# Kernel optimization log

Hardware: AMD Instinct MI355X
Metric: run time of the kernel (lower is better)

Reference implementation:

```python
import jax, jax.numpy as jnp
import numpy as np

B, T, D = 4, 2048, 1024
H = 16
DK = D // H
SCALE = 1.0 / np.sqrt(DK)
EPS_LN = 1e-5
EPS_NORM = 1e-8


def setup_inputs() -> dict:
    key = jax.random.key(0)
    ks = jax.random.split(key, 12)
    gain = 1.0 / np.sqrt(2.0)
    # xavier_uniform bound for square [D, D] weight with gain
    bound = gain * np.sqrt(6.0 / (D + D))

    def w(k):
        return jax.random.uniform(k, (D, D), jnp.float32, -bound, bound)

    return {
        "x": jax.random.normal(ks[0], (B, T, D), jnp.float32),
        "mask": jax.random.bernoulli(ks[1], 0.1, (B, T)),  # True = masked out
        "wq": w(ks[2]), "bq": jnp.zeros((D,), jnp.float32),
        "wk": w(ks[3]), "bk": jnp.zeros((D,), jnp.float32),
        "wv": w(ks[4]), "bv": jnp.zeros((D,), jnp.float32),
        "wo": w(ks[5]), "bo": jnp.zeros((D,), jnp.float32),
        "ln_g": jnp.ones((D,), jnp.float32),
        "ln_b": jnp.zeros((D,), jnp.float32),
    }


def _layernorm(x, g, b):
    mu = jnp.mean(x, axis=-1, keepdims=True)
    var = jnp.var(x, axis=-1, keepdims=True)
    return (x - mu) * jax.lax.rsqrt(var + EPS_LN) * g + b


def _l2norm(x):
    # torch F.normalize: x / clamp_min(||x||_2, eps)
    n = jnp.sqrt(jnp.sum(x * x, axis=-1, keepdims=True))
    return x / jnp.maximum(n, EPS_NORM)


def reference(x, mask, wq, bq, wk, bk, wv, bv, wo, bo, ln_g, ln_b):
    xn = _layernorm(x, ln_g, ln_b)  # q_norm applied to shared input

    def proj(w, bias):
        y = jnp.einsum("btd,ed->bte", xn, w) + bias
        return y.reshape(B, T, H, DK).transpose(0, 2, 1, 3)  # [B,H,T,DK]

    Q = _l2norm(proj(wq, bq))
    K = _l2norm(proj(wk, bk))
    V = proj(wv, bv)

    scores = jnp.einsum("bhqd,bhkd->bhqk", Q, K) * SCALE
    scores = jnp.clip(scores, -10.0, 10.0)
    scores = jnp.where(mask[:, None, None, :], -10000.0, scores)
    scores = scores - jnp.max(scores, axis=-1, keepdims=True)
    attn = jax.nn.softmax(scores, axis=-1)

    out = jnp.einsum("bhqk,bhkd->bhqd", attn, V)
    out = out.transpose(0, 2, 1, 3).reshape(B, T, D)
    out = jnp.einsum("btd,ed->bte", out, wo) + bo
    return out * 0.5
```

## Files before the change

kernel.cpp:

```cpp
#include <hip/hip_runtime.h>
#include <hip/hip_bf16.h>
#include <cstdint>
#include <cstddef>
#include <cstring>

typedef unsigned short u16;
typedef unsigned char u8;
typedef __attribute__((ext_vector_type(8))) short short8;
typedef __attribute__((ext_vector_type(4))) float f32x4;

#define B_    4
#define T_    2048
#define D_    1024
#define H_    16
#define DK_   64
#define QSCALE_ 0.18033688011112042f

__device__ __forceinline__ float bf2f(u16 u) {
    unsigned int x = ((unsigned int)u) << 16;
    float f; __builtin_memcpy(&f, &x, 4); return f;
}
__device__ __forceinline__ u16 f2bf(float f) {
    unsigned int x; __builtin_memcpy(&x, &f, 4);
    x += 0x7fffu + ((x >> 16) & 1u);
    return (u16)(x >> 16);
}

__global__ __launch_bounds__(256) void prep_kernel(
    const u16* __restrict__ x, const u8* __restrict__ m,
    const void* s0, const void* s1, const void* s2, const void* s3,
    const void* s4, const void* s5,
    u16* __restrict__ vecs, float* __restrict__ msk, int* flag, int n)
{
    __shared__ int tot, sbits;
    int tid = threadIdx.x;
    if (tid == 0) { tot = 0; sbits = 0; }
    __syncthreads();
    int cnt = 0;
    for (int i = tid; i < 4096; i += 256) {
        int e = (x[2 * i] >> 7) & 0xFF;
        if (e > 137 || (e >= 1 && e < 97)) cnt++;
    }
    int bits = 0;
    for (int i = tid; i < n; i += 256)
        if (m[i]) bits |= (i & 7);
    for (int o = 1; o < 64; o <<= 1) { cnt += __shfl_xor(cnt, o); bits |= __shfl_xor(bits, o); }
    if ((tid & 63) == 0) { atomicAdd(&tot, cnt); if (bits) atomicOr(&sbits, bits); }
    __syncthreads();
    int f = (tot > 1024) ? 1 : 0;
    if (tid == 0) *flag = f;
    int b = sbits;
    int stride = (b & 1) ? 1 : (b & 2) ? 2 : (b & 4) ? 4 : 8;
    for (int i = tid; i < n; i += 256)
        msk[i] = m[(size_t)i * stride] ? 0.f : 1.f;
    const void* ss[6] = {s0, s1, s2, s3, s4, s5};
    for (int t = 0; t < 6; t++) {
        const void* s = ss[t];
        for (int i = tid; i < 1024; i += 256)
            vecs[t * 1024 + i] = f ? f2bf(((const float*)s)[i]) : ((const u16*)s)[i];
    }
}

__global__ __launch_bounds__(256) void convert_w_kernel(
    const void* s0, const void* s1, const void* s2, const void* s3,
    u16* d0, u16* d1, u16* d2, u16* d3, const int* __restrict__ flag)
{
    const void* s; u16* d;
    if (blockIdx.y == 0)      { s = s0; d = d0; }
    else if (blockIdx.y == 1) { s = s1; d = d1; }
    else if (blockIdx.y == 2) { s = s2; d = d2; }
    else                      { s = s3; d = d3; }
    int i4 = blockIdx.x * 256 + threadIdx.x;
    if (*flag) {
        float4 v = ((const float4*)s)[i4];
        ushort4 o; o.x = f2bf(v.x); o.y = f2bf(v.y); o.z = f2bf(v.z); o.w = f2bf(v.w);
        ((ushort4*)d)[i4] = o;
    } else {
        ((ushort4*)d)[i4] = ((const ushort4*)s)[i4];
    }
}

__global__ __launch_bounds__(256) void ln_kernel(
    const void* __restrict__ x, const u16* __restrict__ g,
    const u16* __restrict__ be, u16* __restrict__ xn, const int* __restrict__ flag)
{
    int row = blockIdx.x;
    int t = threadIdx.x;
    float v[4];
    if (*flag) {
        float4 f4 = ((const float4*)x)[(size_t)row * 256 + t];
        v[0] = f4.x; v[1] = f4.y; v[2] = f4.z; v[3] = f4.w;
    } else {
        ushort4 uv = ((const ushort4*)x)[(size_t)row * 256 + t];
        v[0] = bf2f(uv.x); v[1] = bf2f(uv.y); v[2] = bf2f(uv.z); v[3] = bf2f(uv.w);
    }
    float s = v[0] + v[1] + v[2] + v[3];
    float q = v[0]*v[0] + v[1]*v[1] + v[2]*v[2] + v[3]*v[3];
    for (int o = 1; o < 64; o <<= 1) { s += __shfl_xor(s, o); q += __shfl_xor(q, o); }
    __shared__ float rs[4], rq[4];
    int wv = t >> 6, ln = t & 63;
    if (ln == 0) { rs[wv] = s; rq[wv] = q; }
    __syncthreads();
    s = rs[0] + rs[1] + rs[2] + rs[3];
    q = rq[0] + rq[1] + rq[2] + rq[3];
    float mu   = s * (1.0f / D_);
    float var  = q * (1.0f / D_) - mu * mu;
    float rstd = rsqrtf(var + 1e-5f);
    u16 o4[4];
    for (int i = 0; i < 4; i++) {
        float f = (v[i] - mu) * rstd * bf2f(g[t*4 + i]) + bf2f(be[t*4 + i]);
        o4[i] = f2bf(f);
    }
    ushort4 ov; ov.x = o4[0]; ov.y = o4[1]; ov.z = o4[2]; ov.w = o4[3];
    *(ushort4*)(xn + (size_t)row * D_ + t * 4) = ov;
}

__global__ __launch_bounds__(256) void gemm_bt(
    const u16* __restrict__ A,
    const u16* __restrict__ W0, const u16* __restrict__ W1, const u16* __restrict__ W2,
    const u16* __restrict__ bias_all, int bias_idx0,
    u16* __restrict__ C0, u16* __restrict__ C1, u16* __restrict__ C2,
    float scale, const int* __restrict__ flag, int use_flag, int qkv_mode)
{
    const int K = 1024, N = 1024;
    const u16* W; const u16* bias; u16* C;
    if (blockIdx.z == 0)      { W = W0; bias = bias_all + (size_t)bias_idx0 * 1024;       C = C0; }
    else if (blockIdx.z == 1) { W = W1; bias = bias_all + (size_t)(bias_idx0 + 1) * 1024; C = C1; }
    else                      { W = W2; bias = bias_all + (size_t)(bias_idx0 + 2) * 1024; C = C2; }

    __shared__ u16 As[128 * 32];
    __shared__ u16 Bs[128 * 32];

    int tid  = threadIdx.x;
    int wave = tid >> 6, lane = tid & 63;
    int wm = wave >> 1, wn = wave & 1;
    int quad = lane >> 4, l16 = lane & 15;
    int bm = blockIdx.y * 128, bn = blockIdx.x * 128;

    f32x4 acc[4][4];
    const f32x4 fz = {0.f, 0.f, 0.f, 0.f};
    for (int i = 0; i < 4; i++) for (int j = 0; j < 4; j++) acc[i][j] = fz;

    int srow = lane >> 2;
    int scol = (lane & 3) * 8;
    const u16* gA0 = A + (size_t)(bm + wave * 32 + srow) * K + scol;
    const u16* gB0 = W + (size_t)(bn + wave * 32 + srow) * K + scol;

    for (int k0 = 0; k0 < K; k0 += 32) {
        for (int i = 0; i < 2; i++) {
            __builtin_amdgcn_global_load_lds(
                (const __attribute__((address_space(1))) void*)(gA0 + (size_t)i * 16 * K + k0),
                (__attribute__((address_space(3))) void*)(As + (wave * 32 + i * 16) * 32),
                16, 0, 0);
            __builtin_amdgcn_global_load_lds(
                (const __attribute__((address_space(1))) void*)(gB0 + (size_t)i * 16 * K + k0),
                (__attribute__((address_space(3))) void*)(Bs + (wave * 32 + i * 16) * 32),
                16, 0, 0);
        }
        __syncthreads();
        short8 a[4], b[4];
        for (int i = 0; i < 4; i++)
            a[i] = *(const short8*)(As + (wm * 64 + i * 16 + l16) * 32 + quad * 8);
        for (int j = 0; j < 4; j++)
            b[j] = *(const short8*)(Bs + (wn * 64 + j * 16 + l16) * 32 + quad * 8);
        for (int i = 0; i < 4; i++)
            for (int j = 0; j < 4; j++)
                acc[i][j] = __builtin_amdgcn_mfma_f32_16x16x32_bf16(a[i], b[j], acc[i][j], 0, 0, 0);
        __syncthreads();
    }

    if (qkv_mode) {
        if (blockIdx.z == 2) {
            for (int j = 0; j < 4; j++) {
                int col = bn + wn * 64 + j * 16 + l16;
                int h = col >> 6, d = col & 63;
                float bi = bf2f(bias[col]);
                for (int i = 0; i < 4; i++) {
                    int row0 = bm + wm * 64 + i * 16 + quad * 4;
                    int bq = row0 >> 11, t0 = row0 & 2047;
                    ushort4 pk;
                    pk.x = f2bf(acc[i][j][0] + bi); pk.y = f2bf(acc[i][j][1] + bi);
                    pk.z = f2bf(acc[i][j][2] + bi); pk.w = f2bf(acc[i][j][3] + bi);
                    *(ushort4*)(C + ((size_t)((bq * 16 + h) * 64 + d)) * 2048 + t0) = pk;
                }
            }
        } else {
            float sc2 = (blockIdx.z == 0) ? QSCALE_ : 1.0f;
            float bi[4];
            for (int j = 0; j < 4; j++) bi[j] = bf2f(bias[bn + wn * 64 + j * 16 + l16]);
            for (int i = 0; i < 4; i++) {
                int row0 = bm + wm * 64 + i * 16 + quad * 4;
                for (int r = 0; r < 4; r++) {
                    float v[4]; float s = 0.f;
                    for (int j = 0; j < 4; j++) { v[j] = acc[i][j][r] + bi[j]; s += v[j] * v[j]; }
                    s += __shfl_xor(s, 1); s += __shfl_xor(s, 2);
                    s += __shfl_xor(s, 4); s += __shfl_xor(s, 8);
                    float scl = sc2 / fmaxf(sqrtf(s), 1e-8f);
                    for (int j = 0; j < 4; j++) {
                        int col = bn + wn * 64 + j * 16 + l16;
                        C[(size_t)(row0 + r) * N + col] = f2bf(v[j] * scl);
                    }
                }
            }
        }
        return;
    }

    int f32out = use_flag ? *flag : 0;
    for (int j = 0; j < 4; j++) {
        int col = bn + wn * 64 + j * 16 + l16;
        float bi = bf2f(bias[col]);
        for (int i = 0; i < 4; i++) {
            int row0 = bm + wm * 64 + i * 16 + quad * 4;
            for (int r = 0; r < 4; r++) {
                float o = (acc[i][j][r] + bi) * scale;
                if (f32out) ((float*)C)[(size_t)(row0 + r) * N + col] = o;
                else        C[(size_t)(row0 + r) * N + col] = f2bf(o);
            }
        }
    }
}

__global__ __launch_bounds__(256, 4) void attn_kernel(
    const u16* __restrict__ Q, const u16* __restrict__ Kg,
    const u16* __restrict__ Vt, const float* __restrict__ msk,
    u16* __restrict__ Oout)
{
    __shared__ __align__(16) u16 Ks[64 * 64];
    __shared__ __align__(16) u16 VTs[64 * 64];

    int tid  = threadIdx.x;
    int wave = tid >> 6, lane = tid & 63;
    int quad = lane >> 4, l16 = lane & 15;
    int q0 = blockIdx.x * 128;
    int b  = blockIdx.y >> 4, h = blockIdx.y & 15;
    const size_t base  = (size_t)b * T_ * D_ + h * DK_;
    const size_t vbase = (size_t)((b * 16 + h) * 64) * T_;

    short8 qa[2][2];
    for (int g = 0; g < 2; g++) {
        const u16* qrow = Q + base + (size_t)(q0 + wave * 32 + g * 16 + l16) * D_;
        qa[g][0] = *(const short8*)(qrow + quad * 8);
        qa[g][1] = *(const short8*)(qrow + 32 + quad * 8);
    }

    int sr  = tid >> 3;
    int sc8 = tid & 7;
    const float* mq = msk + b * T_ + quad * 8;

    int r0 = sr, r1 = sr + 32;
    int rho0 = (r0 & 32) + ((r0 >> 2) & 1) * 16 + ((r0 >> 3) & 3) * 4 + (r0 & 3);
    int rho1 = (r1 & 32) + ((r1 >> 2) & 1) * 16 + ((r1 >> 3) & 3) * 4 + (r1 & 3);
    u16* ksw0 = Ks  + rho0 * 64 + ((sc8 ^ (rho0 & 7)) * 8);
    u16* ksw1 = Ks  + rho1 * 64 + ((sc8 ^ (rho1 & 7)) * 8);
    u16* vsw0 = VTs + r0 * 64 + ((sc8 ^ (r0 & 7)) * 8);
    u16* vsw1 = VTs + r1 * 64 + ((sc8 ^ (r1 & 7)) * 8);
    const u16* kg0 = Kg + base + (size_t)r0 * D_ + sc8 * 8;
    const u16* kg1 = Kg + base + (size_t)r1 * D_ + sc8 * 8;
    const u16* vg0 = Vt + vbase + (size_t)r0 * T_ + sc8 * 8;
    const u16* vg1 = Vt + vbase + (size_t)r1 * T_ + sc8 * 8;

    *(short8*)ksw0 = *(const short8*)kg0;
    *(short8*)ksw1 = *(const short8*)kg1;
    *(short8*)vsw0 = *(const short8*)vg0;
    *(short8*)vsw1 = *(const short8*)vg1;
    __syncthreads();

    const u16* kr_lo = Ks + l16 * 64 + ((quad ^ (l16 & 7)) * 8);
    const u16* kr_hi = Ks + l16 * 64 + (((4 + quad) ^ (l16 & 7)) * 8);
    const u16* vr0 = VTs + l16 * 64 + ((quad ^ (l16 & 7)) * 8);
    const u16* vr1 = VTs + l16 * 64 + (((4 + quad) ^ (l16 & 7)) * 8);

    const f32x4 fz = {0.f, 0.f, 0.f, 0.f};
    f32x4 o_acc[2][4];
    for (int g = 0; g < 2; g++) for (int j = 0; j < 4; j++) o_acc[g][j] = fz;
    float rowsum[2] = {0.f, 0.f};

    for (int kt = 0; kt < T_; kt += 64) {
        int ktn = (kt + 64) & (T_ - 1);
        short8 kpre0 = *(const short8*)(kg0 + (size_t)ktn * D_);
        short8 kpre1 = *(const short8*)(kg1 + (size_t)ktn * D_);
        short8 vpre0 = *(const short8*)(vg0 + ktn);
        short8 vpre1 = *(const short8*)(vg1 + ktn);

        for (int j2 = 0; j2 < 2; j2++) {
            unsigned pw[2][4];
            for (int s = 0; s < 2; s++) {
                short8 kb0 = *(const short8*)(kr_lo + (j2 * 32 + s * 16) * 64);
                short8 kb1 = *(const short8*)(kr_hi + (j2 * 32 + s * 16) * 64);
                f32x4 pm = *(const f32x4*)(mq + kt + j2 * 32 + s * 4);
                for (int g = 0; g < 2; g++) {
                    f32x4 s4 = __builtin_amdgcn_mfma_f32_16x16x32_bf16(kb0, qa[g][0], fz, 0, 0, 0);
                    s4       = __builtin_amdgcn_mfma_f32_16x16x32_bf16(kb1, qa[g][1], s4, 0, 0, 0);
                    float p0 = __builtin_exp2f(s4[0]) * pm[0];
                    float p1 = __builtin_exp2f(s4[1]) * pm[1];
                    float p2 = __builtin_exp2f(s4[2]) * pm[2];
                    float p3 = __builtin_exp2f(s4[3]) * pm[3];
                    rowsum[g] += (p0 + p1) + (p2 + p3);
                    __hip_bfloat162 h01 = __float22bfloat162_rn(float2{p0, p1});
                    __hip_bfloat162 h23 = __float22bfloat162_rn(float2{p2, p3});
                    __builtin_memcpy(&pw[g][s * 2],     &h01, 4);
                    __builtin_memcpy(&pw[g][s * 2 + 1], &h23, 4);
                }
            }
            short8 pb[2];
            __builtin_memcpy(&pb[0], &pw[0][0], 16);
            __builtin_memcpy(&pb[1], &pw[1][0], 16);
            const u16* vr = j2 ? vr1 : vr0;
            for (int jd = 0; jd < 4; jd++) {
                short8 vv = *(const short8*)(vr + jd * 16 * 64);
                o_acc[0][jd] = __builtin_amdgcn_mfma_f32_16x16x32_bf16(vv, pb[0], o_acc[0][jd], 0, 0, 0);
                o_acc[1][jd] = __builtin_amdgcn_mfma_f32_16x16x32_bf16(vv, pb[1], o_acc[1][jd], 0, 0, 0);
            }
        }

        __syncthreads();
        *(short8*)ksw0 = kpre0;
        *(short8*)ksw1 = kpre1;
        *(short8*)vsw0 = vpre0;
        *(short8*)vsw1 = vpre1;
        __syncthreads();
    }

    for (int g = 0; g < 2; g++) {
        float l = rowsum[g];
        l += __shfl_xor(l, 16);
        l += __shfl_xor(l, 32);
        float inv = 1.0f / fmaxf(l, 1e-20f);
        size_t orow = base + (size_t)(q0 + wave * 32 + g * 16 + l16) * D_;
        for (int jd = 0; jd < 4; jd++) {
            ushort4 pk;
            pk.x = f2bf(o_acc[g][jd][0] * inv);
            pk.y = f2bf(o_acc[g][jd][1] * inv);
            pk.z = f2bf(o_acc[g][jd][2] * inv);
            pk.w = f2bf(o_acc[g][jd][3] * inv);
            *(ushort4*)(Oout + orow + jd * 16 + quad * 4) = pk;
        }
    }
}

extern "C" void kernel_launch(void* const* d_in, const int* in_sizes, int n_in,
                              void* d_out, int out_size, void* d_ws, size_t ws_size,
                              hipStream_t stream)
{
    const void* x    = d_in[0];
    const u8*   mask = (const u8*)d_in[1];
    const void* wq   = d_in[2];
    const void* bq   = d_in[3];
    const void* wk   = d_in[4];
    const void* bk   = d_in[5];
    const void* wv   = d_in[6];
    const void* bv   = d_in[7];
    const void* wo   = d_in[8];
    const void* bo   = d_in[9];
    const void* lng  = d_in[10];
    const void* lnb  = d_in[11];

    const size_t NTOK = (size_t)B_ * T_;
    u16* xn  = (u16*)d_ws;
    u16* Kb  = xn + NTOK * D_;
    u16* Vtb = Kb + NTOK * D_;
    u16* wqc = Vtb + NTOK * D_;
    u16* wkc = wqc + (size_t)D_ * D_;
    u16* wvc = wkc + (size_t)D_ * D_;
    u16* woc = wvc + (size_t)D_ * D_;
    u16* vecs = woc + (size_t)D_ * D_;
    float* msk = (float*)(vecs + 6 * 1024);
    int* flag = (int*)(msk + 8192);
    u16* Qb  = (u16*)d_out;

    prep_kernel<<<dim3(1), 256, 0, stream>>>((const u16*)x, mask, bq, bk, bv, bo, lng, lnb,
                                             vecs, msk, flag, B_ * T_);
    convert_w_kernel<<<dim3(1024, 4), 256, 0, stream>>>(wq, wk, wv, wo, wqc, wkc, wvc, woc, flag);
    ln_kernel<<<dim3(NTOK), 256, 0, stream>>>(x, vecs + 4 * 1024, vecs + 5 * 1024, xn, flag);
    gemm_bt<<<dim3(8, 64, 3), 256, 0, stream>>>(xn, wqc, wkc, wvc, vecs, 0, Qb, Kb, Vtb, 1.0f, flag, 0, 1);
    attn_kernel<<<dim3(16, 64), 256, 0, stream>>>(Qb, Kb, Vtb, msk, xn);
    gemm_bt<<<dim3(8, 64, 1), 256, 0, stream>>>(xn, woc, woc, woc, vecs, 3, (u16*)d_out, (u16*)d_out, (u16*)d_out, 0.5f, flag, 1, 0);
}
```

Baseline: 374.5 us.

## Load K/V fragments directly from global, fold mask into MFMA accumulator

The attention kernel no longer stages K and V tiles through LDS with double-buffered prefetch and two barriers per step. Each wave now reads its MFMA operand fragments straight from global memory and relies on cache reuse across waves. The mask becomes an additive log-domain bias (-200 or 0) that seeds the score accumulator, replacing a multiply after exp2. Float-to-bf16 packing switches to a perm-based round-half-up. This removes LDS traffic and synchronisation, at the cost of more redundant global/L2 loads, no explicit prefetch, and slightly different rounding.

```diff
diff --git a/kernel.cpp b/kernel.cpp
--- a/kernel.cpp
+++ b/kernel.cpp
@@ -24,6 +24,12 @@
     unsigned int x; __builtin_memcpy(&x, &f, 4);
     x += 0x7fffu + ((x >> 16) & 1u);
     return (u16)(x >> 16);
+}
+__device__ __forceinline__ unsigned pack_bf16_hu(float lo, float hi) {
+    unsigned a, b;
+    __builtin_memcpy(&a, &lo, 4);
+    __builtin_memcpy(&b, &hi, 4);
+    return __builtin_amdgcn_perm(b + 0x8000u, a + 0x8000u, 0x07060302u);
 }
 
 __global__ __launch_bounds__(256) void prep_kernel(
@@ -52,7 +58,7 @@
     int b = sbits;
     int stride = (b & 1) ? 1 : (b & 2) ? 2 : (b & 4) ? 4 : 8;
     for (int i = tid; i < n; i += 256)
-        msk[i] = m[(size_t)i * stride] ? 0.f : 1.f;
+        msk[i] = m[(size_t)i * stride] ? -200.f : 0.f;
     const void* ss[6] = {s0, s1, s2, s3, s4, s5};
     for (int t = 0; t < 6; t++) {
         const void* s = ss[t];
@@ -226,9 +232,6 @@
     const u16* __restrict__ Vt, const float* __restrict__ msk,
     u16* __restrict__ Oout)
 {
-    __shared__ __align__(16) u16 Ks[64 * 64];
-    __shared__ __align__(16) u16 VTs[64 * 64];
-
     int tid  = threadIdx.x;
     int wave = tid >> 6, lane = tid & 63;
     int quad = lane >> 4, l16 = lane & 15;
@@ -244,82 +247,48 @@
         qa[g][1] = *(const short8*)(qrow + 32 + quad * 8);
     }
 
-    int sr  = tid >> 3;
-    int sc8 = tid & 7;
-    const float* mq = msk + b * T_ + quad * 8;
-
-    int r0 = sr, r1 = sr + 32;
-    int rho0 = (r0 & 32) + ((r0 >> 2) & 1) * 16 + ((r0 >> 3) & 3) * 4 + (r0 & 3);
-    int rho1 = (r1 & 32) + ((r1 >> 2) & 1) * 16 + ((r1 >> 3) & 3) * 4 + (r1 & 3);
-    u16* ksw0 = Ks  + rho0 * 64 + ((sc8 ^ (rho0 & 7)) * 8);
-    u16* ksw1 = Ks  + rho1 * 64 + ((sc8 ^ (rho1 & 7)) * 8);
-    u16* vsw0 = VTs + r0 * 64 + ((sc8 ^ (r0 & 7)) * 8);
-    u16* vsw1 = VTs + r1 * 64 + ((sc8 ^ (r1 & 7)) * 8);
-    const u16* kg0 = Kg + base + (size_t)r0 * D_ + sc8 * 8;
-    const u16* kg1 = Kg + base + (size_t)r1 * D_ + sc8 * 8;
-    const u16* vg0 = Vt + vbase + (size_t)r0 * T_ + sc8 * 8;
-    const u16* vg1 = Vt + vbase + (size_t)r1 * T_ + sc8 * 8;
-
-    *(short8*)ksw0 = *(const short8*)kg0;
-    *(short8*)ksw1 = *(const short8*)kg1;
-    *(short8*)vsw0 = *(const short8*)vg0;
-    *(short8*)vsw1 = *(const short8*)vg1;
-    __syncthreads();
-
-    const u16* kr_lo = Ks + l16 * 64 + ((quad ^ (l16 & 7)) * 8);
-    const u16* kr_hi = Ks + l16 * 64 + (((4 + quad) ^ (l16 & 7)) * 8);
-    const u16* vr0 = VTs + l16 * 64 + ((quad ^ (l16 & 7)) * 8);
-    const u16* vr1 = VTs + l16 * 64 + (((4 + quad) ^ (l16 & 7)) * 8);
-
+    int krow = ((l16 & 12) << 1) + (l16 & 3);
+    const u16* kp = Kg + base + (size_t)krow * D_ + quad * 8;
+    const u16* vp = Vt + vbase + (size_t)l16 * T_ + quad * 8;
+    const float* mp = msk + b * T_ + quad * 8;
+
+    f32x4 o_acc[2][4];
     const f32x4 fz = {0.f, 0.f, 0.f, 0.f};
-    f32x4 o_acc[2][4];
     for (int g = 0; g < 2; g++) for (int j = 0; j < 4; j++) o_acc[g][j] = fz;
     float rowsum[2] = {0.f, 0.f};
 
     for (int kt = 0; kt < T_; kt += 64) {
-        int ktn = (kt + 64) & (T_ - 1);
-        short8 kpre0 = *(const short8*)(kg0 + (size_t)ktn * D_);
-        short8 kpre1 = *(const short8*)(kg1 + (size_t)ktn * D_);
-        short8 vpre0 = *(const short8*)(vg0 + ktn);
-        short8 vpre1 = *(const short8*)(vg1 + ktn);
-
         for (int j2 = 0; j2 < 2; j2++) {
             unsigned pw[2][4];
             for (int s = 0; s < 2; s++) {
-                short8 kb0 = *(const short8*)(kr_lo + (j2 * 32 + s * 16) * 64);
-                short8 kb1 = *(const short8*)(kr_hi + (j2 * 32 + s * 16) * 64);
-                f32x4 pm = *(const f32x4*)(mq + kt + j2 * 32 + s * 4);
+                const u16* kb = kp + (size_t)(j2 * 32 + s * 4) * D_;
+                short8 kb0 = *(const short8*)(kb);
+                short8 kb1 = *(const short8*)(kb + 32);
+                f32x4 pm = *(const f32x4*)(mp + j2 * 32 + s * 4);
                 for (int g = 0; g < 2; g++) {
-                    f32x4 s4 = __builtin_amdgcn_mfma_f32_16x16x32_bf16(kb0, qa[g][0], fz, 0, 0, 0);
+                    f32x4 s4 = __builtin_amdgcn_mfma_f32_16x16x32_bf16(kb0, qa[g][0], pm, 0, 0, 0);
                     s4       = __builtin_amdgcn_mfma_f32_16x16x32_bf16(kb1, qa[g][1], s4, 0, 0, 0);
-                    float p0 = __builtin_exp2f(s4[0]) * pm[0];
-                    float p1 = __builtin_exp2f(s4[1]) * pm[1];
-                    float p2 = __builtin_exp2f(s4[2]) * pm[2];
-                    float p3 = __builtin_exp2f(s4[3]) * pm[3];
+                    float p0 = __builtin_exp2f(s4[0]);
+                    float p1 = __builtin_exp2f(s4[1]);
+                    float p2 = __builtin_exp2f(s4[2]);
+                    float p3 = __builtin_exp2f(s4[3]);
                     rowsum[g] += (p0 + p1) + (p2 + p3);
-                    __hip_bfloat162 h01 = __float22bfloat162_rn(float2{p0, p1});
-                    __hip_bfloat162 h23 = __float22bfloat162_rn(float2{p2, p3});
-                    __builtin_memcpy(&pw[g][s * 2],     &h01, 4);
-                    __builtin_memcpy(&pw[g][s * 2 + 1], &h23, 4);
+                    pw[g][s * 2]     = pack_bf16_hu(p0, p1);
+                    pw[g][s * 2 + 1] = pack_bf16_hu(p2, p3);
                 }
             }
             short8 pb[2];
             __builtin_memcpy(&pb[0], &pw[0][0], 16);
             __builtin_memcpy(&pb[1], &pw[1][0], 16);
-            const u16* vr = j2 ? vr1 : vr0;
             for (int jd = 0; jd < 4; jd++) {
-                short8 vv = *(const short8*)(vr + jd * 16 * 64);
+                short8 vv = *(const short8*)(vp + (size_t)jd * 16 * T_ + j2 * 32);
                 o_acc[0][jd] = __builtin_amdgcn_mfma_f32_16x16x32_bf16(vv, pb[0], o_acc[0][jd], 0, 0, 0);
                 o_acc[1][jd] = __builtin_amdgcn_mfma_f32_16x16x32_bf16(vv, pb[1], o_acc[1][jd], 0, 0, 0);
             }
         }
-
-        __syncthreads();
-        *(short8*)ksw0 = kpre0;
-        *(short8*)ksw1 = kpre1;
-        *(short8*)vsw0 = vpre0;
-        *(short8*)vsw1 = vpre1;
-        __syncthreads();
+        kp += (size_t)64 * D_;
+        vp += 64;
+        mp += 64;
     }
 
     for (int g = 0; g < 2; g++) {
```

Result: slower. 494.1 us (+31.9%).
